# Kernel tuning notes

Hardware: AMD Instinct MI355X
Metric: run time of the kernel (lower is better)

Reference implementation:

```python
import jax, jax.numpy as jnp
import numpy as np
from jax import lax
import math

B, C, H, W = 2, 128, 128, 256
K = 3
KK = K * K
AUX = C + 5

def conv2d(x, w, b, pad):
    out = lax.conv_general_dilated(x, w, (1, 1), [(pad, pad), (pad, pad)],
                                   dimension_numbers=('NCHW', 'OIHW', 'NCHW'))
    return out + b[None, :, None, None]

def erp_coord(h, w):
    xs = jnp.linspace(-math.pi, math.pi, w)
    ys = jnp.linspace(-math.pi / 2, math.pi / 2, h)
    theta = jnp.broadcast_to(xs[None, :], (h, w))
    phi = jnp.broadcast_to(ys[:, None], (h, w))
    return jnp.stack([jnp.sin(theta), jnp.cos(theta), jnp.sin(phi), jnp.cos(phi)], 0)[None]

def freq_energy(x, h, w):
    mag = jnp.abs(jnp.fft.rfft2(x, norm='ortho')).mean(1, keepdims=True)
    # bilinear resize (align_corners=False, half-pixel) to (h, w)
    return jax.image.resize(mag, (x.shape[0], 1, h, w), method='linear', antialias=False)

def deform_sample(x, offset):
    # x: (b,c,H,W); offset: (b, 2*KK, H, W)
    b, c, h, w = x.shape
    off = offset.reshape(b, KK, 2, h, w)
    xx = jnp.arange(w, dtype=x.dtype)[None, None, None, :]
    yy = jnp.arange(h, dtype=x.dtype)[None, None, :, None]
    # align_corners=True normalize/unnormalize cancels exactly
    px = xx + off[:, :, 0]  # (b,KK,h,w)
    py = yy + off[:, :, 1]
    x0 = jnp.floor(px).astype(jnp.int32); x1 = x0 + 1
    y0 = jnp.floor(py).astype(jnp.int32); y1 = y0 + 1
    wx1 = px - x0.astype(x.dtype); wx0 = 1.0 - wx1
    wy1 = py - y0.astype(x.dtype); wy0 = 1.0 - wy1
    flat = x.reshape(b, c, h * w)

    def gather(ix, iy):
        valid = ((ix >= 0) & (ix < w) & (iy >= 0) & (iy < h)).astype(x.dtype)
        idx = jnp.clip(iy, 0, h - 1) * w + jnp.clip(ix, 0, w - 1)  # (b,KK,h,w)
        g = jax.vmap(lambda f, i: f[:, i])(flat, idx)  # (b,c,KK,h,w)
        return g * valid[:, None]

    out = (gather(x0, y0) * (wx0 * wy0)[:, None]
           + gather(x1, y0) * (wx1 * wy0)[:, None]
           + gather(x0, y1) * (wx0 * wy1)[:, None]
           + gather(x1, y1) * (wx1 * wy1)[:, None])
    return out.reshape(b, c * KK, h, w)

def setup_inputs() -> dict:
    key = jax.random.key(0)
    ks = jax.random.split(key, 12)
    s = lambda *sh: 1.0 / np.sqrt(np.prod(sh[1:]))
    def unif(k, *sh):
        return jax.random.uniform(k, sh, jnp.float32, -s(*sh), s(*sh))
    return {
        'x': jax.random.normal(ks[0], (B, C, H, W), jnp.float32),
        'offset_w': unif(ks[1], 2 * KK, AUX, 3, 3),
        'offset_b': jnp.zeros((2 * KK,), jnp.float32),
        'gate_w1': unif(ks[2], AUX // 2, AUX, 3, 3),
        'gate_b1': jnp.zeros((AUX // 2,), jnp.float32),
        'gate_w2': unif(ks[3], 1, AUX // 2, 1, 1),
        'gate_b2': jnp.zeros((1,), jnp.float32),
        'base_w': unif(ks[4], C, C, K, K),
        'base_b': jnp.zeros((C,), jnp.float32),
        'def_w': jax.random.normal(ks[5], (C, C, K, K), jnp.float32) * s(C, C, K, K),
        'def_b': jnp.zeros((C,), jnp.float32),
    }

def reference(x, offset_w, offset_b, gate_w1, gate_b1, gate_w2, gate_b2,
              base_w, base_b, def_w, def_b):
    b, c, h, w = x.shape
    coord = jnp.broadcast_to(erp_coord(h, w), (b, 4, h, w)).astype(x.dtype)
    fe = freq_energy(x, h, w)
    aux = jnp.concatenate([x, coord, fe], 1)
    offset = conv2d(aux, offset_w, offset_b, 1)
    g = jax.nn.relu(conv2d(aux, gate_w1, gate_b1, 1))
    gate = jax.nn.sigmoid(conv2d(g, gate_w2, gate_b2, 0))
    y_base = conv2d(x, base_w, base_b, K // 2)
    sampled = deform_sample(x, offset)  # (b, c*KK, h, w)
    y_def = conv2d(sampled, def_w.reshape(c, c * KK, 1, 1), def_b, 0)
    return (1.0 - gate) * y_base + gate * y_def
```

## Files before the change

### kernel.cpp

```cpp
#include <hip/hip_runtime.h>
#include <hip/hip_bf16.h>

#define BB 2
#define CC 128
#define HH 128
#define WW 256
#define HWs (HH*WW)
#define PI_F 3.14159265358979323846f

typedef __attribute__((ext_vector_type(8))) short bf16x8;
typedef __attribute__((ext_vector_type(8))) unsigned short u16x8;
typedef __attribute__((ext_vector_type(4))) float f32x4;
typedef __attribute__((ext_vector_type(2))) float f32x2;

__device__ __forceinline__ ushort f2bf(float f) {
  uint u = __float_as_uint(f);
  u = (u + 0x7fffu + ((u >> 16) & 1u)) >> 16;
  return (ushort)u;
}
__device__ __forceinline__ float bf2f(ushort u) {
  return __uint_as_float(((uint)u) << 16);
}
__device__ __forceinline__ uint comb4(uint u0, uint u1, uint u2, uint u3,
                                      f32x2 g0, f32x2 g1, f32x2 g2, f32x2 g3) {
  f32x2 a0 = (f32x2){__uint_as_float(u0 << 16), __uint_as_float(u0 & 0xffff0000u)};
  f32x2 a1 = (f32x2){__uint_as_float(u1 << 16), __uint_as_float(u1 & 0xffff0000u)};
  f32x2 a2 = (f32x2){__uint_as_float(u2 << 16), __uint_as_float(u2 & 0xffff0000u)};
  f32x2 a3 = (f32x2){__uint_as_float(u3 << 16), __uint_as_float(u3 & 0xffff0000u)};
  f32x2 s = a0 * g0 + a1 * g1 + a2 * g2 + a3 * g3;
  uint ua = __float_as_uint(s.x) + 0x8000u;
  uint ub = __float_as_uint(s.y) + 0x8000u;
  return (ua >> 16) | (ub & 0xffff0000u);
}

__global__ __launch_bounds__(256) void prep_kernel(
    const float* __restrict__ bw, const float* __restrict__ dw,
    const float* __restrict__ ow, const float* __restrict__ gw,
    const float* __restrict__ x,
    ushort* __restrict__ apkF, ushort* __restrict__ apkA,
    ushort* __restrict__ a1, ushort* __restrict__ a2,
    ushort* __restrict__ xt) {
  __shared__ ushort sT[64][128];
  int bid = blockIdx.x;
  int tid = threadIdx.x;
  if (bid >= 284) {
    int blk = bid - 284;
    int wt = blk & 3, h = (blk >> 2) & 127, b = blk >> 9;
    int t = tid;
    const float* xb = x + ((size_t)b * CC * HH + h) * WW;
    ushort* ob = xt + (((size_t)b * HH + h) * WW) * 128;
    {
      int w = t & 63;
      int sw = (w & 7) << 3;
#pragma unroll
      for (int it = 0; it < 4; ++it) {
        int oct = (t >> 6) + it * 4;
        u16x8 v;
#pragma unroll
        for (int j = 0; j < 8; ++j)
          v[j] = f2bf(xb[(size_t)(oct * 8 + j) * HWs + wt * 64 + w]);
        *(u16x8*)&sT[w][(oct << 3) ^ sw] = v;
      }
    }
    __syncthreads();
#pragma unroll
    for (int it = 0; it < 4; ++it) {
      int u = t + it * 256;
      int w = u >> 4, oct = u & 15;
      u16x8 v = *(const u16x8*)&sT[w][(oct << 3) ^ ((w & 7) << 3)];
      *(u16x8*)&ob[(size_t)(wt * 64 + w) * 128 + oct * 8] = v;
    }
    return;
  }
  if (bid < 144) {
    int gid = bid * 256 + tid;
    int lane = gid & 63;
    int kf = (gid >> 6) & 3;
    int mf = (gid >> 8) & 7;
    int chunk = gid >> 11;
    int part = chunk >= 9;
    int tap = part ? chunk - 9 : chunk;
    int m = mf * 16 + (lane & 15);
    int cb = kf * 32 + ((lane >> 4) << 3);
    const float* src = part ? dw : bw;
    ushort* dst = apkF + (size_t)gid * 8;
#pragma unroll
    for (int j = 0; j < 8; ++j)
      dst[j] = f2bf(src[(size_t)m * 1152 + (size_t)(cb + j) * 9 + tap]);
  } else if (bid < 212) {
    int gid = (bid - 144) * 256 + tid;
    if (gid >= 17280) return;
    int lane = gid & 63;
    int kf = (gid >> 6) % 5;
    int mf = (gid / 320) % 6;
    int tap = gid / 1920;
    int m = mf * 16 + (lane & 15);
    int cb = kf * 32 + ((lane >> 4) << 3);
#pragma unroll
    for (int j = 0; j < 8; ++j) {
      int c = cb + j;
      float v = 0.f;
      if (c < 133) {
        if (m < 18) v = ow[(size_t)m * 1197 + c * 9 + tap];
        else if (m < 84) v = gw[(size_t)(m - 18) * 1197 + c * 9 + tap];
      }
      apkA[(size_t)gid * 8 + j] = f2bf(v);
    }
  } else {
    int gid = (bid - 212) * 256 + tid;
    if (gid < 10240) {
      int lane = gid & 63, kf = (gid >> 6) & 7, mf = gid >> 9;
      int m = mf * 16 + (lane & 15);
      int kk0 = kf * 32 + ((lane >> 4) << 3);
#pragma unroll
      for (int j = 0; j < 8; ++j) {
        int kk = kk0 + j;
        float v = 0.f;
        if (m < 129)      { int tt = (m * kk) & 255;         v =  cosf(tt * (PI_F / 128.f)); }
        else if (m < 258) { int tt = ((m - 129) * kk) & 255; v = -sinf(tt * (PI_F / 128.f)); }
        a1[(size_t)gid * 8 + j] = f2bf(v);
      }
    } else if (gid < 18432) {
      int q = gid - 10240;
      int lane = q & 63, kf = (q >> 6) & 7, mf = q >> 9;
      int m = mf * 16 + (lane & 15);
      int g = m & 127;
      int kk0 = kf * 32 + ((lane >> 4) << 3);
#pragma unroll
      for (int j = 0; j < 8; ++j) {
        int kk = kk0 + j;
        int h2 = kk & 127;
        int tt = (g * h2) & 127;
        float ang = tt * (PI_F / 64.f);
        float v = (m < 128) ? ((kk < 128) ? cosf(ang) : sinf(ang))
                            : ((kk < 128) ? -sinf(ang) : cosf(ang));
        a2[(size_t)q * 8 + j] = f2bf(v);
      }
    }
  }
}

__global__ __launch_bounds__(256) void dft1_kernel(const float* __restrict__ x,
    const ushort* __restrict__ a1pk, ushort* __restrict__ F1) {
  int bid = blockIdx.x;
  int bc = bid >> 1, nh = bid & 1;
  int t = threadIdx.x, lane = t & 63, wv = t >> 6;
  int q8 = (lane >> 4) << 3, rq = (lane >> 4) << 2;
  const bf16x8* APK = (const bf16x8*)a1pk;
  ushort* f1b = F1 + (size_t)bc * 36864;
  f32x4 acc[5][4];
#pragma unroll
  for (int i = 0; i < 5; ++i)
#pragma unroll
    for (int n = 0; n < 4; ++n) acc[i][n] = (f32x4){0.f, 0.f, 0.f, 0.f};
  for (int kf = 0; kf < 8; ++kf) {
    bf16x8 av[5];
#pragma unroll
    for (int i = 0; i < 5; ++i)
      av[i] = APK[(size_t)((wv * 5 + i) * 8 + kf) * 64 + lane];
#pragma unroll
    for (int n2 = 0; n2 < 4; ++n2) {
      int nf = nh * 4 + n2;
      int hh = nf * 16 + (lane & 15);
      const float* xp = x + (((size_t)bc * HH + hh) << 8) + kf * 32 + q8;
      float4 xa = *(const float4*)xp;
      float4 xb4 = *(const float4*)(xp + 4);
      bf16x8 bv;
      bv[0] = (short)f2bf(xa.x); bv[1] = (short)f2bf(xa.y);
      bv[2] = (short)f2bf(xa.z); bv[3] = (short)f2bf(xa.w);
      bv[4] = (short)f2bf(xb4.x); bv[5] = (short)f2bf(xb4.y);
      bv[6] = (short)f2bf(xb4.z); bv[7] = (short)f2bf(xb4.w);
#pragma unroll
      for (int i = 0; i < 5; ++i)
        acc[i][n2] = __builtin_amdgcn_mfma_f32_16x16x32_bf16(av[i], bv, acc[i][n2], 0, 0, 0);
    }
  }
#pragma unroll
  for (int n2 = 0; n2 < 4; ++n2) {
    int hh = (nh * 4 + n2) * 16 + (lane & 15);
#pragma unroll
    for (int i = 0; i < 5; ++i) {
#pragma unroll
      for (int r = 0; r < 4; ++r) {
        int m = (wv * 5 + i) * 16 + rq + r;
        if (m < 258) {
          int sel = m >= 129;
          int k = sel ? m - 129 : m;
          f1b[(size_t)k * 256 + sel * 128 + hh] = f2bf(acc[i][n2][r]);
        }
      }
    }
  }
}

__global__ __launch_bounds__(256) void dft2_kernel(const ushort* __restrict__ F1,
    const ushort* __restrict__ a2pk, float* __restrict__ magbuf) {
  int bid = blockIdx.x;
  int bc = bid / 3, ng = bid % 3;
  int t = threadIdx.x, lane = t & 63, wv = t >> 6;
  int q8 = (lane >> 4) << 3, rq = (lane >> 4) << 2;
  const bf16x8* APK = (const bf16x8*)a2pk;
  const ushort* f1b = F1 + (size_t)bc * 36864;
  float* mb = magbuf + (size_t)bc * 18432;
  f32x4 acc[4][3];
#pragma unroll
  for (int i = 0; i < 4; ++i)
#pragma unroll
    for (int n = 0; n < 3; ++n) acc[i][n] = (f32x4){0.f, 0.f, 0.f, 0.f};
  for (int kf = 0; kf < 8; ++kf) {
    bf16x8 av[4];
#pragma unroll
    for (int i = 0; i < 4; ++i) {
      int mf = (i < 2) ? (2 * wv + i) : (2 * wv + (i - 2) + 8);
      av[i] = APK[(size_t)(mf * 8 + kf) * 64 + lane];
    }
#pragma unroll
    for (int n2 = 0; n2 < 3; ++n2) {
      int nf = ng * 3 + n2;
      int krow = nf * 16 + (lane & 15);
      bf16x8 bv = *(const bf16x8*)&f1b[(size_t)krow * 256 + kf * 32 + q8];
#pragma unroll
      for (int i = 0; i < 4; ++i)
        acc[i][n2] = __builtin_amdgcn_mfma_f32_16x16x32_bf16(av[i], bv, acc[i][n2], 0, 0, 0);
    }
  }
#pragma unroll
  for (int n2 = 0; n2 < 3; ++n2) {
    int k = (ng * 3 + n2) * 16 + (lane & 15);
    if (k < 129) {
#pragma unroll
      for (int pr = 0; pr < 2; ++pr) {
#pragma unroll
        for (int r = 0; r < 4; ++r) {
          int g = (2 * wv + pr) * 16 + rq + r;
          float vr = acc[pr][n2][r], vi = acc[pr + 2][n2][r];
          mb[(size_t)g * 144 + k] = sqrtf(vr * vr + vi * vi);
        }
      }
    }
  }
}

__global__ __launch_bounds__(256) void fe_reduce_kernel(const float* __restrict__ magbuf,
    float* __restrict__ fe) {
  int bid = blockIdx.x;
  int i = (bid >> 3) * 256 + threadIdx.x;
  int cq = bid & 7;
  if (i >= 36864) return;
  int k = i % 144;
  int gb = i / 144;
  int g = gb & 127, b = gb >> 7;
  if (k >= 129) return;
  const float* mp = magbuf + (size_t)b * 128 * 18432 + (size_t)g * 144 + k
                  + (size_t)cq * 16 * 18432;
  float s = 0.f;
#pragma unroll
  for (int c = 0; c < 16; ++c) s += mp[(size_t)c * 18432];
  atomicAdd(&fe[((size_t)b * 128 + g) * 129 + k],
            s * (1.0f / (181.01933598375618f * 128.0f)));
}

__global__ __launch_bounds__(256) void aux_conv_kernel(
    const ushort* __restrict__ xt, const float* __restrict__ fe,
    const ushort* __restrict__ apk,
    const float* __restrict__ offset_b, const float* __restrict__ gate_b1,
    const float* __restrict__ w2, const float* __restrict__ b2,
    float* __restrict__ offs, float* __restrict__ gate) {
  __shared__ ushort Bt[64][168];
  __shared__ float gld[66][64];
  __shared__ float2 thS[66];
  __shared__ float2 phS[3];
  __shared__ float feS[3][66];
  int t = threadIdx.x;
  int bid = blockIdx.x;
  int lin = (bid & 7) * 128 + (bid >> 3);
  int bz = lin >> 9;
  int rest = lin & 511;
  int h = rest >> 2, w0 = (rest & 3) << 6;
  int lane = t & 63, wid = t >> 6;
  int wm = wid >> 1, wn = wid & 1;
  int q8 = (lane >> 4) << 3, rq = (lane >> 4) << 2;

  if (t < 66) {
    float th = -PI_F + (float)(w0 + t - 1) * (2.0f * PI_F / 255.0f);
    thS[t] = make_float2(sinf(th), cosf(th));
  }
  if (t < 3) {
    float ph = -0.5f * PI_F + (float)(h + t - 1) * (PI_F / 127.0f);
    phS[t] = make_float2(sinf(ph), cosf(ph));
  }
  if (t < 198) {
    int gyi = t / 66, gxi = t % 66;
    int gy = h + gyi - 1, gx = w0 + gxi - 1;
    float v = 0.f;
    if (gy >= 0 && gy < HH && gx >= 0 && gx < WW) {
      float sxc = ((float)gx + 0.5f) * (129.0f / 256.0f) - 0.5f;
      float fx = floorf(sxc);
      int x0 = (int)fx;
      float fr = sxc - fx;
      int x1 = min(x0 + 1, 128);
      x0 = max(x0, 0);
      const float* fb = fe + ((size_t)bz * 128 + gy) * 129;
      v = fb[x0] * (1.f - fr) + fb[x1] * fr;
    }
    feS[gyi][gxi] = v;
  }

  f32x4 acc[3][2];
#pragma unroll
  for (int i = 0; i < 3; ++i) {
    acc[i][0] = (f32x4){0.f, 0.f, 0.f, 0.f};
    acc[i][1] = (f32x4){0.f, 0.f, 0.f, 0.f};
  }
  int p0 = wn * 32 + (lane & 15), p1 = p0 + 16;
  const bf16x8* APK = (const bf16x8*)apk;
  const ushort* xtb = xt + (size_t)bz * 4194304;

  for (int tap = 0; tap < 9; ++tap) {
    int ky = tap / 3 - 1, kx = tap % 3 - 1;
    int gy = h + ky;
    __syncthreads();
    for (int u = t; u < 1280; u += 256) {
      int oct = u >> 6, p = u & 63;
      int gx = w0 + p + kx;
      bool okp = (gy >= 0) && (gy < HH) && ((unsigned)gx < 256u);
      u16x8 v = (u16x8){0, 0, 0, 0, 0, 0, 0, 0};
      if (oct < 16) {
        if (okp) v = *(const u16x8*)&xtb[((((size_t)gy << 8) + gx) << 7) + (oct << 3)];
      } else if (oct == 16) {
        if (okp) {
          float2 tc = thS[p + kx + 1];
          float2 pc = phS[ky + 1];
          float fv = feS[ky + 1][p + kx + 1];
          v[0] = f2bf(tc.x); v[1] = f2bf(tc.y);
          v[2] = f2bf(pc.x); v[3] = f2bf(pc.y);
          v[4] = f2bf(fv);
        }
      }
      *(u16x8*)&Bt[p][oct << 3] = v;
    }
    __syncthreads();
    int fb = (tap * 6 + wm * 3) * 5;
#pragma unroll
    for (int kf = 0; kf < 5; ++kf) {
      int ko = kf * 32 + q8;
      bf16x8 b0 = *(const bf16x8*)&Bt[p0][ko];
      bf16x8 b1 = *(const bf16x8*)&Bt[p1][ko];
#pragma unroll
      for (int mfi = 0; mfi < 3; ++mfi) {
        bf16x8 av = APK[(size_t)(fb + mfi * 5 + kf) * 64 + lane];
        acc[mfi][0] = __builtin_amdgcn_mfma_f32_16x16x32_bf16(av, b0, acc[mfi][0], 0, 0, 0);
        acc[mfi][1] = __builtin_amdgcn_mfma_f32_16x16x32_bf16(av, b1, acc[mfi][1], 0, 0, 0);
      }
    }
  }
#pragma unroll
  for (int nf = 0; nf < 2; ++nf) {
    int p = wn * 32 + nf * 16 + (lane & 15);
    int w = w0 + p;
#pragma unroll
    for (int mfi = 0; mfi < 3; ++mfi) {
#pragma unroll
      for (int r = 0; r < 4; ++r) {
        int oc = wm * 48 + mfi * 16 + rq + r;
        float v = acc[mfi][nf][r];
        if (oc < 18) {
          offs[((size_t)bz * 18 + oc) * HWs + h * WW + w] = v + offset_b[oc];
        } else if (oc < 84) {
          gld[oc - 18][p] = fmaxf(v + gate_b1[oc - 18], 0.f);
        }
      }
    }
  }
  __syncthreads();
  if (t < 64) {
    float s = b2[0];
    for (int c = 0; c < 66; ++c) s = fmaf(gld[c][t], w2[c], s);
    gate[(size_t)bz * HWs + h * WW + w0 + t] = 1.f / (1.f + expf(-s));
  }
}

__global__ __launch_bounds__(256) void fused_out_kernel(
    const ushort* __restrict__ xt, const float* __restrict__ offsp,
    const ushort* __restrict__ apk,
    const float* __restrict__ base_b, const float* __restrict__ def_b,
    const float* __restrict__ gate, float* __restrict__ out) {
  __shared__ ushort Win[4 * 68 * 64];
  __shared__ ushort Bt[2][64][64];
  __shared__ float gvS[64];
  __shared__ float bbS[128], bdS[128];
  int t = threadIdx.x;
  int bid = blockIdx.x;
  int lin = (bid & 7) * 128 + (bid >> 3);
  int bz = lin >> 9;
  int rest = lin & 511;
  int h = rest >> 2, w0 = (rest & 3) << 6;
  int lane = t & 63, wv = t >> 6;
  int l15 = lane & 15, lg = lane >> 4;
  int rq = lg << 2;
  const ushort* xtb = xt + (size_t)bz * 4194304;
  const bf16x8* APK = (const bf16x8*)apk;
  const u16x8 zv = (u16x8){0, 0, 0, 0, 0, 0, 0, 0};

  if (t < 64) gvS[t] = gate[(size_t)bz * HWs + h * WW + w0 + t];
  else if (t < 192) {
    int c = t - 64;
    bbS[c] = base_b[c];
    bdS[c] = def_b[c];
  }

  int p = t & 63, o4 = t >> 6;
  int mw = w0 + p;
  float oxr[9], oyr[9];
#pragma unroll
  for (int d = 0; d < 9; ++d) {
    oxr[d] = offsp[((size_t)bz * 18 + 2 * d) * HWs + h * WW + mw];
    oyr[d] = offsp[((size_t)bz * 18 + 2 * d + 1) * HWs + h * WW + mw];
  }

  f32x4 accB[2][4], accD[2][4];
#pragma unroll
  for (int mi = 0; mi < 2; ++mi)
#pragma unroll
    for (int nf = 0; nf < 4; ++nf) {
      accB[mi][nf] = (f32x4){0.f, 0.f, 0.f, 0.f};
      accD[mi][nf] = (f32x4){0.f, 0.f, 0.f, 0.f};
    }

  for (int half = 0; half < 2; ++half) {
#pragma unroll
    for (int it = 0; it < 9; ++it) {
      int u = it * 256 + t;
      if (u < 2176) {
        int s = u & 7;
        int c = (u >> 3) % 68;
        int r = u / 544;
        int gy = h - 1 + r, gx = w0 - 2 + c;
        u16x8 v = zv;
        if ((unsigned)gy < 128u && (unsigned)gx < 256u)
          v = *(const u16x8*)&xtb[((((size_t)gy << 8) + gx) << 7) + (half << 6) + (s << 3)];
        *(u16x8*)&Win[((r * 68 + c) << 6) + ((s ^ (c & 7)) << 3)] = v;
      }
    }
    __syncthreads();

    auto stage = [&](int nb, int d) {
      float px = (float)mw + oxr[d], py = (float)h + oyr[d];
      float fx = floorf(px), fy = floorf(py);
      int x0 = (int)fx, y0 = (int)fy;
      float wx1 = px - fx, wy1 = py - fy;
      float wx0 = 1.f - wx1, wy0 = 1.f - wy1;
      int x1 = x0 + 1, y1 = y0 + 1;
      bool vx0 = (unsigned)x0 < 256u, vx1 = (unsigned)x1 < 256u;
      bool vy0 = (unsigned)y0 < 128u, vy1 = (unsigned)y1 < 128u;
      float g0 = (vx0 && vy0) ? wx0 * wy0 : 0.f;
      float g1 = (vx1 && vy0) ? wx1 * wy0 : 0.f;
      float g2 = (vx0 && vy1) ? wx0 * wy1 : 0.f;
      float g3 = (vx1 && vy1) ? wx1 * wy1 : 0.f;
      f32x2 G0 = (f32x2){g0, g0}, G1 = (f32x2){g1, g1};
      f32x2 G2 = (f32x2){g2, g2}, G3 = (f32x2){g3, g3};
      int cx0 = min(max(x0, 0), 255), cx1 = min(max(x1, 0), 255);
      int cy0 = min(max(y0, 0), 127), cy1 = min(max(y1, 0), 127);
      int rx0 = cx0 - w0 + 2, rx1 = cx1 - w0 + 2;
      int ry0 = cy0 - h + 1,  ry1 = cy1 - h + 1;
      bool i00 = ((unsigned)ry0 < 4u) && ((unsigned)rx0 < 68u);
      bool i01 = ((unsigned)ry0 < 4u) && ((unsigned)rx1 < 68u);
      bool i10 = ((unsigned)ry1 < 4u) && ((unsigned)rx0 < 68u);
      bool i11 = ((unsigned)ry1 < 4u) && ((unsigned)rx1 < 68u);
      int wb0 = ((ry0 * 68 + rx0) << 6) ^ ((rx0 & 7) << 3);
      int wb1 = ((ry0 * 68 + rx1) << 6) ^ ((rx1 & 7) << 3);
      int wb2 = ((ry1 * 68 + rx0) << 6) ^ ((rx0 & 7) << 3);
      int wb3 = ((ry1 * 68 + rx1) << 6) ^ ((rx1 & 7) << 3);
      int gb0 = (((cy0 << 8) + cx0) << 7) + (half << 6);
      int gb1 = (((cy0 << 8) + cx1) << 7) + (half << 6);
      int gb2 = (((cy1 << 8) + cx0) << 7) + (half << 6);
      int gb3 = (((cy1 << 8) + cx1) << 7) + (half << 6);
#pragma unroll
      for (int oo = 0; oo < 2; ++oo) {
        int o = o4 + oo * 4;
        int o8 = o << 3;
        uint4 c0, c1, c2, c3;
        if (i00) c0 = *(const uint4*)&Win[wb0 ^ o8];
        else     c0 = *(const uint4*)&xtb[gb0 + o8];
        if (i01) c1 = *(const uint4*)&Win[wb1 ^ o8];
        else     c1 = *(const uint4*)&xtb[gb1 + o8];
        if (i10) c2 = *(const uint4*)&Win[wb2 ^ o8];
        else     c2 = *(const uint4*)&xtb[gb2 + o8];
        if (i11) c3 = *(const uint4*)&Win[wb3 ^ o8];
        else     c3 = *(const uint4*)&xtb[gb3 + o8];
        uint4 r;
        r.x = comb4(c0.x, c1.x, c2.x, c3.x, G0, G1, G2, G3);
        r.y = comb4(c0.y, c1.y, c2.y, c3.y, G0, G1, G2, G3);
        r.z = comb4(c0.z, c1.z, c2.z, c3.z, G0, G1, G2, G3);
        r.w = comb4(c0.w, c1.w, c2.w, c3.w, G0, G1, G2, G3);
        *(uint4*)&Bt[nb][p][(o ^ (p & 7)) << 3] = r;
      }
    };

    stage(0, 0);
    __syncthreads();

    int buf = 0;
    for (int d = 0; d < 9; ++d) {
      int ky = d / 3 - 1, kx = d % 3 - 1;
      int ryB = ky + 1;
#pragma unroll
      for (int kfi = 0; kfi < 2; ++kfi) {
        int kff = half * 2 + kfi;
        int segk = kfi * 4 + lg;
        bf16x8 aB0 = APK[(size_t)((d * 8 + wv) * 4 + kff) * 64 + lane];
        bf16x8 aB1 = APK[(size_t)((d * 8 + wv + 4) * 4 + kff) * 64 + lane];
        bf16x8 aD0 = APK[(size_t)(((9 + d) * 8 + wv) * 4 + kff) * 64 + lane];
        bf16x8 aD1 = APK[(size_t)(((9 + d) * 8 + wv + 4) * 4 + kff) * 64 + lane];
#pragma unroll
        for (int nf = 0; nf < 4; ++nf) {
          int pix = nf * 16 + l15;
          int cxr = pix + kx + 2;
          bf16x8 bB = *(const bf16x8*)&Win[((ryB * 68 + cxr) << 6) + ((segk ^ (cxr & 7)) << 3)];
          bf16x8 bD = *(const bf16x8*)&Bt[buf][pix][(segk ^ (pix & 7)) << 3];
          accB[0][nf] = __builtin_amdgcn_mfma_f32_16x16x32_bf16(aB0, bB, accB[0][nf], 0, 0, 0);
          accB[1][nf] = __builtin_amdgcn_mfma_f32_16x16x32_bf16(aB1, bB, accB[1][nf], 0, 0, 0);
          accD[0][nf] = __builtin_amdgcn_mfma_f32_16x16x32_bf16(aD0, bD, accD[0][nf], 0, 0, 0);
          accD[1][nf] = __builtin_amdgcn_mfma_f32_16x16x32_bf16(aD1, bD, accD[1][nf], 0, 0, 0);
        }
      }
      if (d < 8) stage(buf ^ 1, d + 1);
      __syncthreads();
      buf ^= 1;
    }
    if (half == 0) __syncthreads();
  }

#pragma unroll
  for (int nf = 0; nf < 4; ++nf) {
    int pix = nf * 16 + l15;
    float gv = gvS[pix], go = 1.f - gv;
    int w = w0 + pix;
#pragma unroll
    for (int mi = 0; mi < 2; ++mi) {
      int mf = wv + mi * 4;
#pragma unroll
      for (int r = 0; r < 4; ++r) {
        int oc = mf * 16 + rq + r;
        out[(((size_t)bz * CC + oc) << 15) + h * WW + w] =
            go * (accB[mi][nf][r] + bbS[oc]) + gv * (accD[mi][nf][r] + bdS[oc]);
      }
    }
  }
}

extern "C" void kernel_launch(void* const* d_in, const int* in_sizes, int n_in,
                              void* d_out, int out_size, void* d_ws, size_t ws_size,
                              hipStream_t stream) {
  const float* x        = (const float*)d_in[0];
  const float* offset_w = (const float*)d_in[1];
  const float* offset_b = (const float*)d_in[2];
  const float* gate_w1  = (const float*)d_in[3];
  const float* gate_b1  = (const float*)d_in[4];
  const float* gate_w2  = (const float*)d_in[5];
  const float* gate_b2  = (const float*)d_in[6];
  const float* base_w   = (const float*)d_in[7];
  const float* base_b   = (const float*)d_in[8];
  const float* def_w    = (const float*)d_in[9];
  const float* def_b    = (const float*)d_in[10];
  float* out = (float*)d_out;
  float* ws  = (float*)d_ws;

  float* offsb   = ws;
  float* gatebuf = offsb + 1179648;
  float* fe      = gatebuf + 65536;
  float* magbuf  = fe + 33024;
  ushort* xt     = (ushort*)(magbuf + 4718592);
  ushort* F1     = xt + 16777216;
  ushort* a1pk   = F1 + 9437184;
  ushort* a2pk   = a1pk + 81920;
  ushort* apkF   = a2pk + 65536;
  ushort* apkA   = apkF + 294912;

  hipMemsetAsync(fe, 0, 33024 * sizeof(float), stream);
  prep_kernel<<<1308, 256, 0, stream>>>(base_w, def_w, offset_w, gate_w1, x,
                                        apkF, apkA, a1pk, a2pk, xt);

  dft1_kernel<<<512, 256, 0, stream>>>(x, a1pk, F1);
  dft2_kernel<<<768, 256, 0, stream>>>(F1, a2pk, magbuf);
  fe_reduce_kernel<<<1152, 256, 0, stream>>>(magbuf, fe);

  aux_conv_kernel<<<1024, 256, 0, stream>>>(xt, fe, apkA, offset_b, gate_b1,
                                            gate_w2, gate_b2, offsb, gatebuf);

  fused_out_kernel<<<1024, 256, 0, stream>>>(xt, offsb, apkF, base_b, def_b,
                                             gatebuf, out);
}
```

Measured before the change: 197.1 us.

## Stage 3-row halo window once per channel half in aux conv instead of per tap

The aux conv kernel used to restage a 64x168 B tile in shared memory for each of the 9 taps, with two barriers per tap. It now loads a 3x68 halo window of x once per 64-channel half, using an XOR swizzle against bank conflicts, and builds the coord/freq-energy features once for all taps. Each tap then reads its B fragments straight from the window at shifted offsets. The 1x1 gate conv is also folded into per-lane partial sums before a small shared-memory reduction. The aim is fewer global reloads and barriers, at the cost of slightly different loop structure and more complex indexing.

```diff
diff --git a/kernel.cpp b/kernel.cpp
--- a/kernel.cpp
+++ b/kernel.cpp
@@ -266,11 +266,9 @@
     const float* __restrict__ offset_b, const float* __restrict__ gate_b1,
     const float* __restrict__ w2, const float* __restrict__ b2,
     float* __restrict__ offs, float* __restrict__ gate) {
-  __shared__ ushort Bt[64][168];
-  __shared__ float gld[66][64];
-  __shared__ float2 thS[66];
-  __shared__ float2 phS[3];
-  __shared__ float feS[3][66];
+  __shared__ ushort Win3[3 * 68 * 64];
+  __shared__ ushort coordS[204 * 8];
+  __shared__ float gldP[64][8];
   int t = threadIdx.x;
   int bid = blockIdx.x;
   int lin = (bid & 7) * 128 + (bid >> 3);
@@ -279,21 +277,19 @@
   int h = rest >> 2, w0 = (rest & 3) << 6;
   int lane = t & 63, wid = t >> 6;
   int wm = wid >> 1, wn = wid & 1;
-  int q8 = (lane >> 4) << 3, rq = (lane >> 4) << 2;
-
-  if (t < 66) {
-    float th = -PI_F + (float)(w0 + t - 1) * (2.0f * PI_F / 255.0f);
-    thS[t] = make_float2(sinf(th), cosf(th));
-  }
-  if (t < 3) {
-    float ph = -0.5f * PI_F + (float)(h + t - 1) * (PI_F / 127.0f);
-    phS[t] = make_float2(sinf(ph), cosf(ph));
-  }
-  if (t < 198) {
-    int gyi = t / 66, gxi = t % 66;
-    int gy = h + gyi - 1, gx = w0 + gxi - 1;
-    float v = 0.f;
-    if (gy >= 0 && gy < HH && gx >= 0 && gx < WW) {
+  int l15 = lane & 15, lg = lane >> 4;
+  int rq = lg << 2;
+  const bf16x8* APK = (const bf16x8*)apk;
+  const ushort* xtb = xt + (size_t)bz * 4194304;
+  const bf16x8 zvb = (bf16x8){0, 0, 0, 0, 0, 0, 0, 0};
+
+  if (t < 204) {
+    int r = t / 68, c = t - r * 68;
+    int gy = h - 1 + r, gx = w0 - 2 + c;
+    u16x8 v = (u16x8){0, 0, 0, 0, 0, 0, 0, 0};
+    if ((unsigned)gy < 128u && (unsigned)gx < 256u) {
+      float th = -PI_F + (float)gx * (2.0f * PI_F / 255.0f);
+      float ph = -0.5f * PI_F + (float)gy * (PI_F / 127.0f);
       float sxc = ((float)gx + 0.5f) * (129.0f / 256.0f) - 0.5f;
       float fx = floorf(sxc);
       int x0 = (int)fx;
@@ -301,9 +297,12 @@
       int x1 = min(x0 + 1, 128);
       x0 = max(x0, 0);
       const float* fb = fe + ((size_t)bz * 128 + gy) * 129;
-      v = fb[x0] * (1.f - fr) + fb[x1] * fr;
-    }
-    feS[gyi][gxi] = v;
+      float fv = fb[x0] * (1.f - fr) + fb[x1] * fr;
+      v[0] = f2bf(sinf(th)); v[1] = f2bf(cosf(th));
+      v[2] = f2bf(sinf(ph)); v[3] = f2bf(cosf(ph));
+      v[4] = f2bf(fv);
+    }
+    *(u16x8*)&coordS[t * 8] = v;
   }
 
   f32x4 acc[3][2];
@@ -312,51 +311,58 @@
     acc[i][0] = (f32x4){0.f, 0.f, 0.f, 0.f};
     acc[i][1] = (f32x4){0.f, 0.f, 0.f, 0.f};
   }
-  int p0 = wn * 32 + (lane & 15), p1 = p0 + 16;
-  const bf16x8* APK = (const bf16x8*)apk;
-  const ushort* xtb = xt + (size_t)bz * 4194304;
-
-  for (int tap = 0; tap < 9; ++tap) {
-    int ky = tap / 3 - 1, kx = tap % 3 - 1;
-    int gy = h + ky;
+  int p0 = wn * 32 + l15, p1 = p0 + 16;
+
+  for (int half = 0; half < 2; ++half) {
+    if (half) __syncthreads();
+    for (int it = 0; it < 7; ++it) {
+      int u = it * 256 + t;
+      if (u < 1632) {
+        int s = u & 7;
+        int c = (u >> 3) % 68;
+        int r = u / 544;
+        int gy = h - 1 + r, gx = w0 - 2 + c;
+        u16x8 v = (u16x8){0, 0, 0, 0, 0, 0, 0, 0};
+        if ((unsigned)gy < 128u && (unsigned)gx < 256u)
+          v = *(const u16x8*)&xtb[((((size_t)gy << 8) + gx) << 7) + (half << 6) + (s << 3)];
+        *(u16x8*)&Win3[((r * 68 + c) << 6) + ((s ^ (c & 7)) << 3)] = v;
+      }
+    }
     __syncthreads();
-    for (int u = t; u < 1280; u += 256) {
-      int oct = u >> 6, p = u & 63;
-      int gx = w0 + p + kx;
-      bool okp = (gy >= 0) && (gy < HH) && ((unsigned)gx < 256u);
-      u16x8 v = (u16x8){0, 0, 0, 0, 0, 0, 0, 0};
-      if (oct < 16) {
-        if (okp) v = *(const u16x8*)&xtb[((((size_t)gy << 8) + gx) << 7) + (oct << 3)];
-      } else if (oct == 16) {
-        if (okp) {
-          float2 tc = thS[p + kx + 1];
-          float2 pc = phS[ky + 1];
-          float fv = feS[ky + 1][p + kx + 1];
-          v[0] = f2bf(tc.x); v[1] = f2bf(tc.y);
-          v[2] = f2bf(pc.x); v[3] = f2bf(pc.y);
-          v[4] = f2bf(fv);
+
+    for (int tap = 0; tap < 9; ++tap) {
+      int ky = tap / 3 - 1, kx = tap % 3 - 1;
+      int rr = ky + 1;
+      int c0 = p0 + kx + 2, c1 = p1 + kx + 2;
+      int nkf = half ? 3 : 2;
+      for (int kfi = 0; kfi < nkf; ++kfi) {
+        bf16x8 b0, b1;
+        int kf;
+        if (kfi < 2) {
+          kf = half * 2 + kfi;
+          int s = kfi * 4 + lg;
+          b0 = *(const bf16x8*)&Win3[((rr * 68 + c0) << 6) + ((s ^ (c0 & 7)) << 3)];
+          b1 = *(const bf16x8*)&Win3[((rr * 68 + c1) << 6) + ((s ^ (c1 & 7)) << 3)];
+        } else {
+          kf = 4;
+          b0 = (lg == 0) ? *(const bf16x8*)&coordS[(rr * 68 + c0) * 8] : zvb;
+          b1 = (lg == 0) ? *(const bf16x8*)&coordS[(rr * 68 + c1) * 8] : zvb;
         }
-      }
-      *(u16x8*)&Bt[p][oct << 3] = v;
-    }
-    __syncthreads();
-    int fb = (tap * 6 + wm * 3) * 5;
-#pragma unroll
-    for (int kf = 0; kf < 5; ++kf) {
-      int ko = kf * 32 + q8;
-      bf16x8 b0 = *(const bf16x8*)&Bt[p0][ko];
-      bf16x8 b1 = *(const bf16x8*)&Bt[p1][ko];
-#pragma unroll
-      for (int mfi = 0; mfi < 3; ++mfi) {
-        bf16x8 av = APK[(size_t)(fb + mfi * 5 + kf) * 64 + lane];
-        acc[mfi][0] = __builtin_amdgcn_mfma_f32_16x16x32_bf16(av, b0, acc[mfi][0], 0, 0, 0);
-        acc[mfi][1] = __builtin_amdgcn_mfma_f32_16x16x32_bf16(av, b1, acc[mfi][1], 0, 0, 0);
-      }
-    }
-  }
+        int fb = (tap * 6 + wm * 3) * 5 + kf;
+#pragma unroll
+        for (int mfi = 0; mfi < 3; ++mfi) {
+          bf16x8 av = APK[(size_t)(fb + mfi * 5) * 64 + lane];
+          acc[mfi][0] = __builtin_amdgcn_mfma_f32_16x16x32_bf16(av, b0, acc[mfi][0], 0, 0, 0);
+          acc[mfi][1] = __builtin_amdgcn_mfma_f32_16x16x32_bf16(av, b1, acc[mfi][1], 0, 0, 0);
+        }
+      }
+    }
+  }
+
+  float gp[2] = {0.f, 0.f};
 #pragma unroll
   for (int nf = 0; nf < 2; ++nf) {
-    int p = wn * 32 + nf * 16 + (lane & 15);
+    int p = wn * 32 + nf * 16 + l15;
     int w = w0 + p;
 #pragma unroll
     for (int mfi = 0; mfi < 3; ++mfi) {
@@ -367,15 +373,18 @@
         if (oc < 18) {
           offs[((size_t)bz * 18 + oc) * HWs + h * WW + w] = v + offset_b[oc];
         } else if (oc < 84) {
-          gld[oc - 18][p] = fmaxf(v + gate_b1[oc - 18], 0.f);
+          gp[nf] += w2[oc - 18] * fmaxf(v + gate_b1[oc - 18], 0.f);
         }
       }
     }
   }
+  gldP[p0][wm * 4 + lg] = gp[0];
+  gldP[p1][wm * 4 + lg] = gp[1];
   __syncthreads();
   if (t < 64) {
     float s = b2[0];
-    for (int c = 0; c < 66; ++c) s = fmaf(gld[c][t], w2[c], s);
+#pragma unroll
+    for (int i = 0; i < 8; ++i) s += gldP[t][i];
     gate[(size_t)bz * HWs + h * WW + w0 + t] = 1.f / (1.f + expf(-s));
   }
 }
```

Result: no change. 195.5 us (median of 2 runs) (-0.8%).
